# Kernel optimization log

Hardware: AMD Instinct MI355X
Metric: run time of the kernel (lower is better)

The kernel has to match this reference:

```python
import jax, jax.numpy as jnp
import numpy as np

NUM_WIRES = 12
NUM_LAYERS = 4
NUM_OUTPUTS = 4
BATCH = 1024
DIM = 2 ** NUM_WIRES


def _apply_1q(psi, U, w):
    # psi: (B, 2**n) complex64; U: (2,2) shared or (B,2,2) per-sample; wire 0 = most significant.
    B = psi.shape[0]
    L = 2 ** w
    R = DIM // (2 * L)
    psi = psi.reshape(B, L, 2, R)
    if U.ndim == 2:
        psi = jnp.einsum('ij,bljr->blir', U, psi)
    else:
        psi = jnp.einsum('bij,bljr->blir', U, psi)
    return psi.reshape(B, DIM)


def _cnot(psi, c, t):
    # CNOT(control=c, target=t): flip target amplitudes in the control=1 half.
    B = psi.shape[0]
    psi = psi.reshape((B,) + (2,) * NUM_WIRES)
    a0 = jax.lax.index_in_dim(psi, 0, c + 1, keepdims=True)
    a1 = jax.lax.index_in_dim(psi, 1, c + 1, keepdims=True)
    a1 = jnp.flip(a1, axis=t + 1)
    psi = jnp.concatenate([a0, a1], axis=c + 1)
    return psi.reshape(B, DIM)


def _rot(phi, theta, omega):
    # PennyLane Rot(phi, theta, omega) = RZ(omega) @ RY(theta) @ RZ(phi)
    c = jnp.cos(theta / 2)
    s = jnp.sin(theta / 2)
    u00 = jnp.exp(-0.5j * (phi + omega)) * c
    u01 = -jnp.exp(0.5j * (phi - omega)) * s
    u10 = jnp.exp(-0.5j * (phi - omega)) * s
    u11 = jnp.exp(0.5j * (phi + omega)) * c
    return jnp.stack([jnp.stack([u00, u01]), jnp.stack([u10, u11])]).astype(jnp.complex64)


def _circuit(inputs, weights):
    B = inputs.shape[0]
    psi = jnp.zeros((B, DIM), jnp.complex64).at[:, 0].set(1.0)
    # AngleEmbedding with rotation 'Y': RY(pi/2 * x_w) on wire w (per-sample angles)
    theta = (jnp.pi / 2) * inputs  # (B, n)
    c = jnp.cos(theta / 2)
    s = jnp.sin(theta / 2)
    for w in range(NUM_WIRES):
        U = jnp.stack([jnp.stack([c[:, w], -s[:, w]], -1),
                       jnp.stack([s[:, w], c[:, w]], -1)], -2).astype(jnp.complex64)  # (B,2,2)
        psi = _apply_1q(psi, U, w)
    # StronglyEntanglingLayers: Rot on every wire, then ring of CNOTs with range r
    for l in range(NUM_LAYERS):
        for w in range(NUM_WIRES):
            psi = _apply_1q(psi, _rot(weights[l, w, 0], weights[l, w, 1], weights[l, w, 2]), w)
        r = (l % (NUM_WIRES - 1)) + 1
        for w in range(NUM_WIRES):
            psi = _cnot(psi, w, (w + r) % NUM_WIRES)
    # expval(PauliZ) on the first NUM_OUTPUTS wires
    probs = jnp.abs(psi) ** 2  # (B, DIM) float32
    idx = jnp.arange(DIM)
    shifts = NUM_WIRES - 1 - jnp.arange(NUM_OUTPUTS)
    signs = (1.0 - 2.0 * ((idx[None, :] >> shifts[:, None]) & 1)).astype(probs.dtype)  # (NOUT, DIM)
    return probs @ signs.T  # (B, NUM_OUTPUTS)


def setup_inputs() -> dict:
    key = jax.random.key(0)
    k1, k2 = jax.random.split(key)
    inputs = jax.random.uniform(k1, (BATCH, NUM_WIRES), jnp.float32, -1.0, 1.0)
    weights = jax.random.uniform(k2, (NUM_LAYERS, NUM_WIRES, 3), jnp.float32, 0.0, 2.0 * np.pi)
    return {"inputs": inputs, "weights": weights}


def reference(inputs, weights):
    return _circuit(inputs, weights)
```

## Files before the change

kernel.cpp:

```cpp
#include <hip/hip_runtime.h>
#include <hip/hip_bf16.h>

#define NW 12
#define DIM 4096
#define NL 4
#define NGATE 48
#define NOUT 4
#define TPB 256

typedef float f32x2 __attribute__((ext_vector_type(2)));
typedef float f32x4 __attribute__((ext_vector_type(4)));
typedef unsigned u32x4 __attribute__((ext_vector_type(4)));
typedef short short8 __attribute__((ext_vector_type(8)));

constexpr int pcnt(unsigned x){ return __builtin_popcount(x); }
constexpr int msbp(unsigned x){ return x ? 31-__builtin_clz(x) : -1; }
constexpr unsigned ring_fwd(unsigned x,int r){
  for(int w=0;w<NW;++w){ int c=NW-1-w,t=NW-1-((w+r)%NW); x^=((x>>c)&1u)<<t; } return x;
}
constexpr unsigned ring_rev(unsigned x,int r){
  for(int w=NW-1;w>=0;--w){ int c=NW-1-w,t=NW-1-((w+r)%NW); x^=((x>>c)&1u)<<t; } return x;
}
struct Mat { unsigned col[12]; };
constexpr unsigned apply_cols(const Mat&M, unsigned v){
  unsigned r=0; for(int j=0;j<12;++j) if((v>>j)&1u) r^=M.col[j]; return r;
}
constexpr unsigned apply_rows(const unsigned* rows, unsigned v){
  unsigned r=0; for(int i=0;i<12;++i) r|=(unsigned)(pcnt(rows[i]&v)&1)<<i; return r;
}
constexpr bool invert_rows(const Mat&M, unsigned* ri_out){
  unsigned rb[12]={}, ri[12]={};
  for(int i=0;i<12;++i){ unsigned r=0; for(int j=0;j<12;++j) r|=((M.col[j]>>i)&1u)<<j; rb[i]=r; ri[i]=1u<<i; }
  for(int c=0;c<12;++c){
    int piv=-1; for(int r=c;r<12;++r) if((rb[r]>>c)&1u){piv=r;break;}
    if(piv<0) return false;
    unsigned t=rb[c]; rb[c]=rb[piv]; rb[piv]=t; t=ri[c]; ri[c]=ri[piv]; ri[piv]=t;
    for(int r=0;r<12;++r) if(r!=c&&((rb[r]>>c)&1u)){ rb[r]^=rb[c]; ri[r]^=ri[c]; }
  }
  for(int i=0;i<12;++i) ri_out[i]=ri[i];
  return true;
}
constexpr int nullspace4(const unsigned* A0, unsigned* out){
  unsigned A[4]={}; for(int i=0;i<4;++i) A[i]=A0[i];
  int rank=0; int pivc[4]={-1,-1,-1,-1};
  for(int c=0;c<12&&rank<4;++c){
    int piv=-1; for(int r=rank;r<4;++r) if((A[r]>>c)&1u){piv=r;break;}
    if(piv<0) continue;
    unsigned t=A[rank];A[rank]=A[piv];A[piv]=t;
    for(int r=0;r<4;++r) if(r!=rank&&((A[r]>>c)&1u)) A[r]^=A[rank];
    pivc[rank]=c; ++rank;
  }
  if(rank!=4) return -1;
  bool ispiv[12]={};
  for(int r=0;r<4;++r) ispiv[pivc[r]]=true;
  int cnt=0;
  for(int f=0;f<12;++f) if(!ispiv[f]){
    unsigned v=1u<<f;
    for(int r=0;r<4;++r) if((A[r]>>f)&1u) v|=1u<<pivc[r];
    out[cnt++]=v;
  }
  return cnt;
}
struct Ech { unsigned r[12]; int lead[12]; int n; };
constexpr unsigned ech_red(const Ech&e, unsigned v){
  int mv=msbp(v);
  for(int i=0;i<e.n&&v;++i) if(e.lead[i]==mv){ v^=e.r[i]; mv=msbp(v); }
  return v;
}
constexpr void ech_add(Ech&e, unsigned v){
  int l=msbp(v); int pos=e.n;
  while(pos>0&&e.lead[pos-1]<l){ e.r[pos]=e.r[pos-1]; e.lead[pos]=e.lead[pos-1]; --pos; }
  e.r[pos]=v; e.lead[pos]=l; e.n+=1;
}

struct Circ {
  unsigned M[NL][12]; unsigned RM[NL][12]; unsigned MR[NOUT];
};
constexpr Circ make_circ(){
  Circ C{};
  unsigned cols[12]={}, icols[12]={};
  for(int p=0;p<12;++p){ cols[p]=1u<<p; icols[p]=1u<<p; }
  for(int l=0;l<NL;++l){
    for(int w=0;w<NW;++w){
      int p=NW-1-w;
      C.M[l][w]=icols[p];
      unsigned r=0; for(int j=0;j<12;++j) r|=((cols[j]>>p)&1u)<<j;
      C.RM[l][w]=r;
    }
    int rr=(l%(NW-1))+1;
    for(int j=0;j<12;++j) cols[j]=ring_fwd(cols[j],rr);
    unsigned nic[12]={};
    for(int p=0;p<12;++p){
      unsigned y=ring_rev(1u<<p,rr), v=0;
      for(int q=0;q<12;++q) if((y>>q)&1u) v^=icols[q];
      nic[p]=v;
    }
    for(int p=0;p<12;++p) icols[p]=nic[p];
  }
  for(int o=0;o<NOUT;++o){
    int p=NW-1-o; unsigned r=0;
    for(int j=0;j<12;++j) r|=((cols[j]>>p)&1u)<<j;
    C.MR[o]=r;
  }
  return C;
}

constexpr unsigned amap(unsigned v){ return (v>>8)*2048u + (v&255u)*8u; }

struct Plan2 {
  unsigned SCOLt[8];
  unsigned SK16[16];
  unsigned TM;
  unsigned WBC[12][8], WOFF[12][16];
  unsigned RBC[12][8], ROFF[12][16];
  unsigned SRt[NOUT], KP[NOUT];
  bool ok;
};

constexpr Plan2 make_plan2(){
  Plan2 P{}; P.ok=true;
  constexpr Circ C = make_circ();
  const int SIGl[8] = {0,1,2,3,10,11,6,7};
  Mat Bprev{}; for(int j=0;j<12;++j) Bprev.col[j]=1u<<j;
  for(int g=0; g<12; ++g){
    int l=g/3, j0=(g%3)*4;
    unsigned mi[4]={}, rmi[4]={};
    for(int i=0;i<4;++i){ mi[i]=C.M[l][j0+i]; rmi[i]=C.RM[l][j0+i]; }
    unsigned u[8]={};
    if(nullspace4(rmi,u)!=8){ P.ok=false; return P; }
    unsigned binv[12]={};
    if(!invert_rows(Bprev,binv)){ P.ok=false; return P; }
    for(int s=0;s<8;++s) u[s]=apply_rows(binv,u[s]);
    Mat Bg{};
    for(int j=0;j<8;++j) Bg.col[j]=apply_cols(Bprev,u[j]);
    for(int i=0;i<4;++i) Bg.col[8+i]=mi[i];
    unsigned tinv[12]={};
    if(!invert_rows(Bg,tinv)){ P.ok=false; return P; }
    for(int i=0;i<4;++i)
      for(int j=0;j<12;++j){
        int want=(j==8+i)?1:0;
        if((pcnt(Bg.col[j]&rmi[i])&1)!=want){ P.ok=false; return P; }
      }
    if(g==0){
      for(int j=0;j<8;++j) P.SCOLt[j]=Bg.col[SIGl[j]];
      for(int idx=0;idx<16;++idx){
        unsigned v=0;
        if((idx>>2)&1) v^=Bg.col[4];
        if((idx>>2)&2) v^=Bg.col[5];
        if(idx&1) v^=Bg.col[8];
        if(idx&2) v^=Bg.col[9];
        P.SK16[idx]=v; P.TM|=v;
      }
    } else {
      unsigned rk[4]={};
      for(int i=0;i<4;++i){
        rk[i]=apply_rows(binv,mi[i]);
        if(apply_cols(Bprev,rk[i])!=mi[i]){ P.ok=false; return P; }
      }
      unsigned s2b[6]={u[0],u[1],u[2],u[3],rk[2],rk[3]};
      unsigned rows[12]={}; int nr=0;
      Ech P1{},P2{},ER{};
      for(int pick=0;pick<4;++pick){
        unsigned fx=0, fy=0;
        const int b1s[6]={0,1,2,3,10,11};
        for(int ii=0;ii<6;++ii){
          unsigned f=1u<<b1s[ii];
          unsigned p1=(f&15u)|(((f>>10)&3u)<<4);
          if(ech_red(P1,p1)){ fx=f; break; }
        }
        for(int bb=0;bb<12;++bb){
          unsigned f=1u<<bb, p2=0;
          for(int i2=0;i2<6;++i2) p2|=(unsigned)(pcnt(f&s2b[i2])&1)<<i2;
          if(ech_red(P2,p2)){ fy=f; break; }
        }
        if(!fx||!fy){ P.ok=false; return P; }
        unsigned cand[3]={fx,fy,fx^fy};
        unsigned chosen=0, cp1=0, cp2=0;
        for(int ci=0; ci<3 && !chosen; ++ci){
          unsigned f=cand[ci];
          unsigned p1=(f&15u)|(((f>>10)&3u)<<4);
          unsigned p2=0; for(int i2=0;i2<6;++i2) p2|=(unsigned)(pcnt(f&s2b[i2])&1)<<i2;
          if(ech_red(P1,p1)&&ech_red(P2,p2)){ chosen=f; cp1=p1; cp2=p2; }
        }
        if(!chosen){ P.ok=false; return P; }
        { unsigned v1=ech_red(P1,cp1); ech_add(P1,v1); }
        { unsigned v2=ech_red(P2,cp2); ech_add(P2,v2); }
        { unsigned vr=ech_red(ER,chosen); if(!vr){ P.ok=false; return P; } ech_add(ER,vr); }
        rows[nr++]=chosen;
      }
      for(int bb=0;bb<12 && nr<12;++bb){
        unsigned vr=ech_red(ER,1u<<bb); if(!vr) continue;
        ech_add(ER,vr); rows[nr++]=1u<<bb;
      }
      if(nr!=12){ P.ok=false; return P; }
      unsigned PhiCol[12]={};
      for(int j=0;j<12;++j){
        unsigned v=0;
        for(int i=0;i<12;++i) v|=(unsigned)((rows[i]>>j)&1u)<<i;
        PhiCol[j]=v;
      }
      unsigned PhiM[12]={};
      for(int j=0;j<12;++j){
        unsigned src=(j<8)? u[j] : rk[j-8];
        unsigned v=0;
        for(int q2=0;q2<12;++q2) if((src>>q2)&1u) v^=PhiCol[q2];
        PhiM[j]=v;
      }
      for(int j=0;j<8;++j){
        P.WBC[g][j]=amap(PhiCol[SIGl[j]]);
        P.RBC[g][j]=amap(PhiM[SIGl[j]]);
      }
      for(int idx=0;idx<16;++idx){
        unsigned wv=0, rv=0;
        if((idx>>2)&1){ wv^=PhiCol[4]; rv^=PhiM[4]; }
        if((idx>>2)&2){ wv^=PhiCol[5]; rv^=PhiM[5]; }
        if(idx&1){ wv^=PhiCol[8]; rv^=PhiM[8]; }
        if(idx&2){ wv^=PhiCol[9]; rv^=PhiM[9]; }
        P.WOFF[g][idx]=amap(wv); P.ROFF[g][idx]=amap(rv);
      }
    }
    Bprev=Bg;
  }
  for(int o=0;o<NOUT;++o){
    unsigned sr=0;
    for(int j=0;j<12;++j) sr|=(unsigned)(pcnt(Bprev.col[j]&C.MR[o])&1)<<j;
    unsigned srt=0;
    const int SIGl2[8] = {0,1,2,3,10,11,6,7};
    for(int j=0;j<8;++j) srt|=((sr>>SIGl2[j])&1u)<<j;
    P.SRt[o]=srt;
    unsigned kp=0;
    for(int idx=0;idx<16;++idx){
      int T=idx>>2, q=idx&3;
      unsigned bit=(((sr>>4)&1u)&(unsigned)(T&1))^(((sr>>5)&1u)&(unsigned)((T>>1)&1))
                  ^(((sr>>8)&1u)&(unsigned)(q&1))^(((sr>>9)&1u)&(unsigned)((q>>1)&1));
      kp|=bit<<idx;
    }
    P.KP[o]=kp;
  }
  return P;
}

constexpr Plan2 PL2C = make_plan2();
static_assert(PL2C.ok, "plan2 failed");
__device__ constexpr Plan2 PL2 = PL2C;

__device__ __forceinline__ void gate_coeffs(const float* __restrict__ wts, int gi, float* o){
  const float* w = wts + gi*3;
  float st,ct;  sincosf(0.5f*w[1],&st,&ct);
  float sap,cap; sincosf(0.5f*(w[0]+w[2]),&sap,&cap);
  float sam,cam; sincosf(0.5f*(w[0]-w[2]),&sam,&cam);
  o[0]= cap*ct; o[1]=-sap*ct;
  o[2]=-cam*st; o[3]=-sam*st;
  o[4]= cam*st; o[5]=-sam*st;
  o[6]= cap*ct; o[7]= sap*ct;
}
__device__ __forceinline__ unsigned cvtpk(float a, float b){
  unsigned r; asm("v_cvt_pk_bf16_f32 %0, %1, %2" : "=v"(r) : "v"(a), "v"(b)); return r;
}
__device__ __forceinline__ void split2(float x, float& hf, float& lf){
  __hip_bfloat16 hb = __float2bfloat16(x);
  hf = __bfloat162float(hb);
  lf = x - hf;
}
__device__ __forceinline__ void pkhl(float x0, float x1, unsigned& hw_out, unsigned& lw_out){
  unsigned hw = cvtpk(x0, x1);
  float h0 = __uint_as_float(hw << 16);
  float h1 = __uint_as_float(hw & 0xffff0000u);
  lw_out = cvtpk(x0 - h0, x1 - h1);
  hw_out = hw;
}

__device__ __forceinline__ void do_mfma_T(const float2& v0, const float2& v1,
                                          const float2& v2, const float2& v3,
                                          const short8* AF, f32x4& cr_o, f32x4& ci_o){
  unsigned h0,l0,h1,l1;
  pkhl(v0.x, v1.x, h0, l0);
  pkhl(v2.x, v3.x, h1, l1);
  u32x4 bu; bu.x=h0; bu.y=h1; bu.z=l0; bu.w=l1;
  short8 Br = __builtin_bit_cast(short8, bu);
  pkhl(v0.y, v1.y, h0, l0);
  pkhl(v2.y, v3.y, h1, l1);
  u32x4 cu; cu.x=h0; cu.y=h1; cu.z=l0; cu.w=l1;
  short8 Bi = __builtin_bit_cast(short8, cu);
  const f32x4 z = {0.f,0.f,0.f,0.f};
  f32x4 cr = __builtin_amdgcn_mfma_f32_16x16x32_bf16(AF[0], Br, z, 0,0,0);
  cr = __builtin_amdgcn_mfma_f32_16x16x32_bf16(AF[1], Br, cr, 0,0,0);
  cr = __builtin_amdgcn_mfma_f32_16x16x32_bf16(AF[4], Bi, cr, 0,0,0);
  cr = __builtin_amdgcn_mfma_f32_16x16x32_bf16(AF[5], Bi, cr, 0,0,0);
  f32x4 ci = __builtin_amdgcn_mfma_f32_16x16x32_bf16(AF[2], Br, z, 0,0,0);
  ci = __builtin_amdgcn_mfma_f32_16x16x32_bf16(AF[3], Br, ci, 0,0,0);
  ci = __builtin_amdgcn_mfma_f32_16x16x32_bf16(AF[0], Bi, ci, 0,0,0);
  ci = __builtin_amdgcn_mfma_f32_16x16x32_bf16(AF[1], Bi, ci, 0,0,0);
  cr_o = cr; ci_o = ci;
}

__global__ void coeff2_kernel(const float* __restrict__ wts, unsigned short* __restrict__ gfrag){
  const int g = blockIdx.x;
  const int tid = threadIdx.x;
  const int m = tid & 15, rp = tid >> 4;
  const int s = rp >> 1, reg = rp & 1;
  const int r0 = 4*s + 2*reg, r1 = r0 + 1;
  const int l = g/3, j0 = (g%3)*4;
  float ur0=1.f, ui0=0.f, ur1=1.f, ui1=0.f;
  #pragma unroll
  for(int i=0;i<4;++i){
    float o[8]; gate_coeffs(wts, l*NW + j0 + i, o);
    int mb=(m>>i)&1, rb0=(r0>>i)&1, rb1=(r1>>i)&1;
    float er=o[(mb*2+rb0)*2], ei=o[(mb*2+rb0)*2+1];
    float tr=ur0*er-ui0*ei, ti=ur0*ei+ui0*er; ur0=tr; ui0=ti;
    er=o[(mb*2+rb1)*2]; ei=o[(mb*2+rb1)*2+1];
    tr=ur1*er-ui1*ei; ti=ur1*ei+ui1*er; ur1=tr; ui1=ti;
  }
  float ur0h,ur0l,ur1h,ur1l, ui0h,ui0l,ui1h,ui1l;
  split2(ur0,ur0h,ur0l); split2(ur1,ur1h,ur1l);
  split2(ui0,ui0h,ui0l); split2(ui1,ui1h,ui1l);
  unsigned Urh=cvtpk(ur0h,ur1h), Url=cvtpk(ur0l,ur1l);
  unsigned Uih=cvtpk(ui0h,ui1h), Uil=cvtpk(ui0l,ui1l);
  unsigned nUih=Uih^0x80008000u, nUil=Uil^0x80008000u;
  const int lane = s*16 + m;
  unsigned p0[6]={Urh,Url,Uih,Uil,nUih,nUil};
  unsigned p1[6]={Url,Urh,Uil,Uih,nUil,nUih};
  #pragma unroll
  for(int f=0; f<6; ++f){
    unsigned* fp = (unsigned*)((char*)gfrag + ((size_t)((g*6+f)*64 + lane))*16);
    fp[reg] = p0[f];
    fp[2+reg] = p1[f];
  }
}

#define LUT_BYTES (11*32*8)
__global__ __launch_bounds__(TPB,4)
void vqc_mfma(const float* __restrict__ inp, const unsigned short* __restrict__ gfrag,
              float* __restrict__ out){
  __shared__ __align__(16) char smem[DIM*8 + LUT_BYTES];
  float* cs = (float*)smem; float* ss = cs+NW; float* red = cs+2*NW;
  char* ampc = smem;
  uint2* blut = (uint2*)(smem + DIM*8);
  const int t = threadIdx.x, b = blockIdx.x, l = t&63;
  if(t < NW){
    float x = inp[b*NW+t];
    float s,c; sincosf(0.78539816339744830962f*x,&s,&c);
    cs[t]=c; ss[t]=s;
  }
  for(int e=t; e<11*32; e+=TPB){
    int gg=(e>>5)+1, idx=e&31;
    int hi=idx>>4, nib=idx&15;
    unsigned wv=0, rv=0;
    #pragma unroll
    for(int j=0;j<4;++j){
      if((nib>>j)&1){
        int jj = j + (hi?4:0);
        wv ^= PL2.WBC[gg][jj];
        rv ^= PL2.RBC[gg][jj];
      }
    }
    blut[e]=make_uint2(wv,rv);
  }
  __syncthreads();
  float ctm[12], stm[12];
  #pragma unroll
  for(int p=0;p<12;++p){ ctm[p]=cs[11-p]; stm[p]=ss[11-p]; }
  unsigned sigb=0;
  #pragma unroll
  for(int j=0;j<8;++j) sigb ^= ((t>>j)&1u)? PL2.SCOLt[j] : 0u;
  float pbase=1.f;
  #pragma unroll
  for(int p=0;p<12;++p)
    if(!((PL2C.TM>>p)&1u))
      pbase *= ((sigb>>p)&1u)? stm[p] : ctm[p];

  short8 AF[6];
  #pragma unroll
  for(int f=0; f<6; ++f)
    AF[f] = *(const short8*)((const char*)gfrag + ((size_t)(f*64 + l))*16);

  f32x4 Cr[4], Ci[4];

  {
    #pragma unroll
    for(int T=0;T<4;++T){
      float vv[4];
      #pragma unroll
      for(int rq=0;rq<4;++rq){
        unsigned sig = sigb ^ PL2.SK16[T*4+rq];
        float pk=pbase;
        #pragma unroll
        for(int p=0;p<12;++p)
          if((PL2C.TM>>p)&1u)
            pk *= ((sig>>p)&1u)? stm[p] : ctm[p];
        vv[rq]=pk;
      }
      float2 v0=make_float2(vv[0],0.f), v1=make_float2(vv[1],0.f);
      float2 v2=make_float2(vv[2],0.f), v3=make_float2(vv[3],0.f);
      __builtin_amdgcn_s_setprio(1);
      do_mfma_T(v0,v1,v2,v3, AF, Cr[T], Ci[T]);
      __builtin_amdgcn_s_setprio(0);
    }
    #pragma unroll
    for(int f=0; f<6; ++f)
      AF[f] = *(const short8*)((const char*)gfrag + ((size_t)((6+f)*64 + l))*16);
  }

  #pragma unroll 1
  for(int g=1; g<12; ++g){
    const uint2* bl = blut + (g-1)*32;
    uint2 lo = bl[t&15];
    uint2 hi = bl[16 + (t>>4)];
    unsigned wbase = lo.x ^ hi.x;
    unsigned rbase = lo.y ^ hi.y;
    __syncthreads();
    #pragma unroll
    for(int idx=0; idx<16; ++idx){
      const int T=idx>>2, q=idx&3;
      *(float2*)(ampc + (wbase ^ PL2.WOFF[g][idx])) = make_float2(Cr[T][q], Ci[T][q]);
    }
    __syncthreads();
    #pragma unroll
    for(int T=0;T<4;++T){
      float2 v0 = *(const float2*)(ampc + (rbase ^ PL2.ROFF[g][T*4+0]));
      float2 v1 = *(const float2*)(ampc + (rbase ^ PL2.ROFF[g][T*4+1]));
      float2 v2 = *(const float2*)(ampc + (rbase ^ PL2.ROFF[g][T*4+2]));
      float2 v3 = *(const float2*)(ampc + (rbase ^ PL2.ROFF[g][T*4+3]));
      __builtin_amdgcn_s_setprio(1);
      do_mfma_T(v0,v1,v2,v3, AF, Cr[T], Ci[T]);
      __builtin_amdgcn_s_setprio(0);
    }
    if(g<11){
      #pragma unroll
      for(int f=0; f<6; ++f)
        AF[f] = *(const short8*)((const char*)gfrag + ((size_t)(((g+1)*6+f)*64 + l))*16);
    }
  }

  float acc[NOUT]={0.f,0.f,0.f,0.f};
  float sg[NOUT];
  #pragma unroll
  for(int o=0;o<NOUT;++o)
    sg[o] = (__popc((unsigned)t & PL2.SRt[o])&1)? -1.f : 1.f;
  #pragma unroll
  for(int idx=0; idx<16; ++idx){
    const int T=idx>>2, q=idx&3;
    float pr = Cr[T][q]*Cr[T][q] + Ci[T][q]*Ci[T][q];
    #pragma unroll
    for(int o=0;o<NOUT;++o){
      const bool kp = (PL2C.KP[o]>>idx)&1;
      float f = sg[o]*pr;
      acc[o] += kp? -f : f;
    }
  }
  #pragma unroll
  for(int o=0;o<NOUT;++o)
    #pragma unroll
    for(int off=32; off>0; off>>=1)
      acc[o] += __shfl_down(acc[o], off);
  __syncthreads();
  const int wv=t>>6, ln=t&63;
  if(ln==0){
    #pragma unroll
    for(int o=0;o<NOUT;++o) red[wv*NOUT+o]=acc[o];
  }
  __syncthreads();
  if(t<NOUT)
    out[b*NOUT+t] = red[0*NOUT+t]+red[1*NOUT+t]+red[2*NOUT+t]+red[3*NOUT+t];
}

extern "C" void kernel_launch(void* const* d_in, const int* in_sizes, int n_in,
                              void* d_out, int out_size, void* d_ws, size_t ws_size,
                              hipStream_t stream) {
  const float* inp=(const float*)d_in[0];
  const float* wts=(const float*)d_in[1];
  float* outp=(float*)d_out;
  const int B = in_sizes[0]/NW;
  unsigned short* gfrag=(unsigned short*)d_ws;
  coeff2_kernel<<<12,128,0,stream>>>(wts,gfrag);
  vqc_mfma<<<B,TPB,0,stream>>>(inp,gfrag,outp);
}
```

Measured before the change: 39.74 us.

## Double threads per sample so each thread holds 8 amplitudes instead of 16

Raises the block size from 256 to 512 threads and remaps the state-vector partition so each thread owns 8 amplitudes (2 MFMA tiles) instead of 16. The constexpr plan tables gain a ninth thread-index column and shrink the per-thread offset tables. The LDS address map becomes linear, which drops the previous bank-spreading layout, and the cached cos/sin register arrays are removed. This aims for more parallelism and fewer registers per thread, at the cost of more waves per block and more barrier participants per gate group.

```diff
diff --git a/kernel.cpp b/kernel.cpp
--- a/kernel.cpp
+++ b/kernel.cpp
@@ -6,7 +6,7 @@
 #define NL 4
 #define NGATE 48
 #define NOUT 4
-#define TPB 256
+#define TPB 512
 
 typedef float f32x2 __attribute__((ext_vector_type(2)));
 typedef float f32x4 __attribute__((ext_vector_type(4)));
@@ -105,14 +105,15 @@
   return C;
 }
 
-constexpr unsigned amap(unsigned v){ return (v>>8)*2048u + (v&255u)*8u; }
+
+constexpr unsigned amap(unsigned v){ return v*8u; }
 
 struct Plan2 {
-  unsigned SCOLt[8];
-  unsigned SK16[16];
+  unsigned SCOLt[9];
+  unsigned SK8[8];
   unsigned TM;
-  unsigned WBC[12][8], WOFF[12][16];
-  unsigned RBC[12][8], ROFF[12][16];
+  unsigned WBC[12][9], WOFF[12][8];
+  unsigned RBC[12][9], ROFF[12][8];
   unsigned SRt[NOUT], KP[NOUT];
   bool ok;
 };
@@ -120,7 +121,7 @@
 constexpr Plan2 make_plan2(){
   Plan2 P{}; P.ok=true;
   constexpr Circ C = make_circ();
-  const int SIGl[8] = {0,1,2,3,10,11,6,7};
+  const int SIGp[9] = {0,1,2,3,10,11,5,6,7};
   Mat Bprev{}; for(int j=0;j<12;++j) Bprev.col[j]=1u<<j;
   for(int g=0; g<12; ++g){
     int l=g/3, j0=(g%3)*4;
@@ -142,14 +143,13 @@
         if((pcnt(Bg.col[j]&rmi[i])&1)!=want){ P.ok=false; return P; }
       }
     if(g==0){
-      for(int j=0;j<8;++j) P.SCOLt[j]=Bg.col[SIGl[j]];
-      for(int idx=0;idx<16;++idx){
+      for(int j=0;j<9;++j) P.SCOLt[j]=Bg.col[SIGp[j]];
+      for(int idx=0;idx<8;++idx){
         unsigned v=0;
-        if((idx>>2)&1) v^=Bg.col[4];
-        if((idx>>2)&2) v^=Bg.col[5];
-        if(idx&1) v^=Bg.col[8];
-        if(idx&2) v^=Bg.col[9];
-        P.SK16[idx]=v; P.TM|=v;
+        if(idx&1) v^=Bg.col[4];
+        if(idx&2) v^=Bg.col[8];
+        if(idx&4) v^=Bg.col[9];
+        P.SK8[idx]=v; P.TM|=v;
       }
     } else {
       unsigned rk[4]={};
@@ -206,16 +206,15 @@
         for(int q2=0;q2<12;++q2) if((src>>q2)&1u) v^=PhiCol[q2];
         PhiM[j]=v;
       }
-      for(int j=0;j<8;++j){
-        P.WBC[g][j]=amap(PhiCol[SIGl[j]]);
-        P.RBC[g][j]=amap(PhiM[SIGl[j]]);
-      }
-      for(int idx=0;idx<16;++idx){
+      for(int j=0;j<9;++j){
+        P.WBC[g][j]=amap(PhiCol[SIGp[j]]);
+        P.RBC[g][j]=amap(PhiM[SIGp[j]]);
+      }
+      for(int idx=0;idx<8;++idx){
         unsigned wv=0, rv=0;
-        if((idx>>2)&1){ wv^=PhiCol[4]; rv^=PhiM[4]; }
-        if((idx>>2)&2){ wv^=PhiCol[5]; rv^=PhiM[5]; }
-        if(idx&1){ wv^=PhiCol[8]; rv^=PhiM[8]; }
-        if(idx&2){ wv^=PhiCol[9]; rv^=PhiM[9]; }
+        if(idx&1){ wv^=PhiCol[4]; rv^=PhiM[4]; }
+        if(idx&2){ wv^=PhiCol[8]; rv^=PhiM[8]; }
+        if(idx&4){ wv^=PhiCol[9]; rv^=PhiM[9]; }
         P.WOFF[g][idx]=amap(wv); P.ROFF[g][idx]=amap(rv);
       }
     }
@@ -225,14 +224,15 @@
     unsigned sr=0;
     for(int j=0;j<12;++j) sr|=(unsigned)(pcnt(Bprev.col[j]&C.MR[o])&1)<<j;
     unsigned srt=0;
-    const int SIGl2[8] = {0,1,2,3,10,11,6,7};
-    for(int j=0;j<8;++j) srt|=((sr>>SIGl2[j])&1u)<<j;
+    const int SIGp2[9] = {0,1,2,3,10,11,5,6,7};
+    for(int j=0;j<9;++j) srt|=((sr>>SIGp2[j])&1u)<<j;
     P.SRt[o]=srt;
     unsigned kp=0;
-    for(int idx=0;idx<16;++idx){
-      int T=idx>>2, q=idx&3;
-      unsigned bit=(((sr>>4)&1u)&(unsigned)(T&1))^(((sr>>5)&1u)&(unsigned)((T>>1)&1))
-                  ^(((sr>>8)&1u)&(unsigned)(q&1))^(((sr>>9)&1u)&(unsigned)((q>>1)&1));
+    for(int idx=0;idx<8;++idx){
+      int T=idx&1, q=idx>>1;
+      unsigned bit = (((sr>>4)&1u)&(unsigned)T)
+                   ^ (((sr>>8)&1u)&(unsigned)(q&1))
+                   ^ (((sr>>9)&1u)&(unsigned)((q>>1)&1));
       kp|=bit<<idx;
     }
     P.KP[o]=kp;
@@ -269,7 +269,6 @@
   lw_out = cvtpk(x0 - h0, x1 - h1);
   hw_out = hw;
 }
-
 __device__ __forceinline__ void do_mfma_T(const float2& v0, const float2& v1,
                                           const float2& v2, const float2& v3,
                                           const short8* AF, f32x4& cr_o, f32x4& ci_o){
@@ -329,7 +328,7 @@
 }
 
 #define LUT_BYTES (11*32*8)
-__global__ __launch_bounds__(TPB,4)
+__global__ __launch_bounds__(TPB,8)
 void vqc_mfma(const float* __restrict__ inp, const unsigned short* __restrict__ gfrag,
               float* __restrict__ out){
   __shared__ __align__(16) char smem[DIM*8 + LUT_BYTES];
@@ -357,38 +356,35 @@
     blut[e]=make_uint2(wv,rv);
   }
   __syncthreads();
-  float ctm[12], stm[12];
-  #pragma unroll
-  for(int p=0;p<12;++p){ ctm[p]=cs[11-p]; stm[p]=ss[11-p]; }
   unsigned sigb=0;
   #pragma unroll
-  for(int j=0;j<8;++j) sigb ^= ((t>>j)&1u)? PL2.SCOLt[j] : 0u;
+  for(int j=0;j<9;++j) sigb ^= ((t>>j)&1u)? PL2.SCOLt[j] : 0u;
   float pbase=1.f;
   #pragma unroll
   for(int p=0;p<12;++p)
     if(!((PL2C.TM>>p)&1u))
-      pbase *= ((sigb>>p)&1u)? stm[p] : ctm[p];
+      pbase *= ((sigb>>p)&1u)? ss[11-p] : cs[11-p];
 
   short8 AF[6];
   #pragma unroll
   for(int f=0; f<6; ++f)
     AF[f] = *(const short8*)((const char*)gfrag + ((size_t)(f*64 + l))*16);
 
-  f32x4 Cr[4], Ci[4];
+  f32x4 Cr[2], Ci[2];
 
   {
     #pragma unroll
-    for(int T=0;T<4;++T){
+    for(int T=0;T<2;++T){
       float vv[4];
       #pragma unroll
-      for(int rq=0;rq<4;++rq){
-        unsigned sig = sigb ^ PL2.SK16[T*4+rq];
+      for(int q=0;q<4;++q){
+        unsigned sig = sigb ^ PL2.SK8[T | (q<<1)];
         float pk=pbase;
         #pragma unroll
         for(int p=0;p<12;++p)
           if((PL2C.TM>>p)&1u)
-            pk *= ((sig>>p)&1u)? stm[p] : ctm[p];
-        vv[rq]=pk;
+            pk *= ((sig>>p)&1u)? ss[11-p] : cs[11-p];
+        vv[q]=pk;
       }
       float2 v0=make_float2(vv[0],0.f), v1=make_float2(vv[1],0.f);
       float2 v2=make_float2(vv[2],0.f), v3=make_float2(vv[3],0.f);
@@ -405,22 +401,26 @@
   for(int g=1; g<12; ++g){
     const uint2* bl = blut + (g-1)*32;
     uint2 lo = bl[t&15];
-    uint2 hi = bl[16 + (t>>4)];
+    uint2 hi = bl[16 + ((t>>4)&15)];
     unsigned wbase = lo.x ^ hi.x;
     unsigned rbase = lo.y ^ hi.y;
+    if(t & 256){
+      wbase ^= PL2.WBC[g][8];
+      rbase ^= PL2.RBC[g][8];
+    }
     __syncthreads();
     #pragma unroll
-    for(int idx=0; idx<16; ++idx){
-      const int T=idx>>2, q=idx&3;
+    for(int idx=0; idx<8; ++idx){
+      const int T=idx&1, q=idx>>1;
       *(float2*)(ampc + (wbase ^ PL2.WOFF[g][idx])) = make_float2(Cr[T][q], Ci[T][q]);
     }
     __syncthreads();
     #pragma unroll
-    for(int T=0;T<4;++T){
-      float2 v0 = *(const float2*)(ampc + (rbase ^ PL2.ROFF[g][T*4+0]));
-      float2 v1 = *(const float2*)(ampc + (rbase ^ PL2.ROFF[g][T*4+1]));
-      float2 v2 = *(const float2*)(ampc + (rbase ^ PL2.ROFF[g][T*4+2]));
-      float2 v3 = *(const float2*)(ampc + (rbase ^ PL2.ROFF[g][T*4+3]));
+    for(int T=0;T<2;++T){
+      float2 v0 = *(const float2*)(ampc + (rbase ^ PL2.ROFF[g][(0<<1)|T]));
+      float2 v1 = *(const float2*)(ampc + (rbase ^ PL2.ROFF[g][(1<<1)|T]));
+      float2 v2 = *(const float2*)(ampc + (rbase ^ PL2.ROFF[g][(2<<1)|T]));
+      float2 v3 = *(const float2*)(ampc + (rbase ^ PL2.ROFF[g][(3<<1)|T]));
       __builtin_amdgcn_s_setprio(1);
       do_mfma_T(v0,v1,v2,v3, AF, Cr[T], Ci[T]);
       __builtin_amdgcn_s_setprio(0);
@@ -438,8 +438,8 @@
   for(int o=0;o<NOUT;++o)
     sg[o] = (__popc((unsigned)t & PL2.SRt[o])&1)? -1.f : 1.f;
   #pragma unroll
-  for(int idx=0; idx<16; ++idx){
-    const int T=idx>>2, q=idx&3;
+  for(int idx=0; idx<8; ++idx){
+    const int T=idx&1, q=idx>>1;
     float pr = Cr[T][q]*Cr[T][q] + Ci[T][q]*Ci[T][q];
     #pragma unroll
     for(int o=0;o<NOUT;++o){
@@ -460,8 +460,12 @@
     for(int o=0;o<NOUT;++o) red[wv*NOUT+o]=acc[o];
   }
   __syncthreads();
-  if(t<NOUT)
-    out[b*NOUT+t] = red[0*NOUT+t]+red[1*NOUT+t]+red[2*NOUT+t]+red[3*NOUT+t];
+  if(t<NOUT){
+    float s=0.f;
+    #pragma unroll
+    for(int w=0;w<8;++w) s += red[w*NOUT+t];
+    out[b*NOUT+t] = s;
+  }
 }
 
 extern "C" void kernel_launch(void* const* d_in, const int* in_sizes, int n_in,
```

Result: slower. 43.15 us (+8.6%).

## Process two batch samples per block to share gate fragments and overlap MFMA chains

Applied to the files above, without the earlier changes.

Each block now simulates two samples with separate LDS amplitude buffers, interleaving their shuffles and MFMA chains. Gate fragments loaded from global memory are reused across both samples, and one barrier per gate is removed. The cost is double the registers and LDS per block, lowered launch bounds, and half as many blocks, which reduces how many waves are in flight.

```diff
diff --git a/kernel.cpp b/kernel.cpp
--- a/kernel.cpp
+++ b/kernel.cpp
@@ -269,7 +269,6 @@
   lw_out = cvtpk(x0 - h0, x1 - h1);
   hw_out = hw;
 }
-
 __device__ __forceinline__ void do_mfma_T(const float2& v0, const float2& v1,
                                           const float2& v2, const float2& v3,
                                           const short8* AF, f32x4& cr_o, f32x4& ci_o){
@@ -329,18 +328,25 @@
 }
 
 #define LUT_BYTES (11*32*8)
-__global__ __launch_bounds__(TPB,4)
+__global__ __launch_bounds__(TPB,2)
 void vqc_mfma(const float* __restrict__ inp, const unsigned short* __restrict__ gfrag,
               float* __restrict__ out){
-  __shared__ __align__(16) char smem[DIM*8 + LUT_BYTES];
-  float* cs = (float*)smem; float* ss = cs+NW; float* red = cs+2*NW;
-  char* ampc = smem;
-  uint2* blut = (uint2*)(smem + DIM*8);
+  __shared__ __align__(16) char smem[2*DIM*8 + LUT_BYTES];
+  __shared__ float csb[2][NW], ssb[2][NW];
+  __shared__ float red[2][4][NOUT];
+  char* ampA = smem;
+  char* ampB = smem + DIM*8;
+  uint2* blut = (uint2*)(smem + 2*DIM*8);
   const int t = threadIdx.x, b = blockIdx.x, l = t&63;
   if(t < NW){
-    float x = inp[b*NW+t];
+    float x = inp[(2*b)*NW+t];
     float s,c; sincosf(0.78539816339744830962f*x,&s,&c);
-    cs[t]=c; ss[t]=s;
+    csb[0][t]=c; ssb[0][t]=s;
+  } else if(t >= 64 && t < 64+NW){
+    int tt = t-64;
+    float x = inp[(2*b+1)*NW+tt];
+    float s,c; sincosf(0.78539816339744830962f*x,&s,&c);
+    csb[1][tt]=c; ssb[1][tt]=s;
   }
   for(int e=t; e<11*32; e+=TPB){
     int gg=(e>>5)+1, idx=e&31;
@@ -357,26 +363,24 @@
     blut[e]=make_uint2(wv,rv);
   }
   __syncthreads();
-  float ctm[12], stm[12];
-  #pragma unroll
-  for(int p=0;p<12;++p){ ctm[p]=cs[11-p]; stm[p]=ss[11-p]; }
   unsigned sigb=0;
   #pragma unroll
   for(int j=0;j<8;++j) sigb ^= ((t>>j)&1u)? PL2.SCOLt[j] : 0u;
-  float pbase=1.f;
-  #pragma unroll
-  for(int p=0;p<12;++p)
-    if(!((PL2C.TM>>p)&1u))
-      pbase *= ((sigb>>p)&1u)? stm[p] : ctm[p];
 
   short8 AF[6];
   #pragma unroll
   for(int f=0; f<6; ++f)
     AF[f] = *(const short8*)((const char*)gfrag + ((size_t)(f*64 + l))*16);
 
-  f32x4 Cr[4], Ci[4];
-
-  {
+  f32x4 CrA[4], CiA[4], CrB[4], CiB[4];
+
+  #pragma unroll
+  for(int s=0; s<2; ++s){
+    float pbase=1.f;
+    #pragma unroll
+    for(int p=0;p<12;++p)
+      if(!((PL2C.TM>>p)&1u))
+        pbase *= ((sigb>>p)&1u)? ssb[s][11-p] : csb[s][11-p];
     #pragma unroll
     for(int T=0;T<4;++T){
       float vv[4];
@@ -387,19 +391,20 @@
         #pragma unroll
         for(int p=0;p<12;++p)
           if((PL2C.TM>>p)&1u)
-            pk *= ((sig>>p)&1u)? stm[p] : ctm[p];
+            pk *= ((sig>>p)&1u)? ssb[s][11-p] : csb[s][11-p];
         vv[rq]=pk;
       }
       float2 v0=make_float2(vv[0],0.f), v1=make_float2(vv[1],0.f);
       float2 v2=make_float2(vv[2],0.f), v3=make_float2(vv[3],0.f);
       __builtin_amdgcn_s_setprio(1);
-      do_mfma_T(v0,v1,v2,v3, AF, Cr[T], Ci[T]);
+      if(s==0) do_mfma_T(v0,v1,v2,v3, AF, CrA[T], CiA[T]);
+      else     do_mfma_T(v0,v1,v2,v3, AF, CrB[T], CiB[T]);
       __builtin_amdgcn_s_setprio(0);
     }
-    #pragma unroll
-    for(int f=0; f<6; ++f)
-      AF[f] = *(const short8*)((const char*)gfrag + ((size_t)((6+f)*64 + l))*16);
-  }
+  }
+  #pragma unroll
+  for(int f=0; f<6; ++f)
+    AF[f] = *(const short8*)((const char*)gfrag + ((size_t)((6+f)*64 + l))*16);
 
   #pragma unroll 1
   for(int g=1; g<12; ++g){
@@ -408,21 +413,36 @@
     uint2 hi = bl[16 + (t>>4)];
     unsigned wbase = lo.x ^ hi.x;
     unsigned rbase = lo.y ^ hi.y;
-    __syncthreads();
     #pragma unroll
     for(int idx=0; idx<16; ++idx){
       const int T=idx>>2, q=idx&3;
-      *(float2*)(ampc + (wbase ^ PL2.WOFF[g][idx])) = make_float2(Cr[T][q], Ci[T][q]);
+      *(float2*)(ampA + (wbase ^ PL2.WOFF[g][idx])) = make_float2(CrA[T][q], CiA[T][q]);
     }
     __syncthreads();
+    float2 ra[16];
+    #pragma unroll
+    for(int idx=0; idx<16; ++idx)
+      ra[idx] = *(const float2*)(ampA + (rbase ^ PL2.ROFF[g][idx]));
+    #pragma unroll
+    for(int idx=0; idx<16; ++idx){
+      const int T=idx>>2, q=idx&3;
+      *(float2*)(ampB + (wbase ^ PL2.WOFF[g][idx])) = make_float2(CrB[T][q], CiB[T][q]);
+    }
+    __syncthreads();
+    float2 rb[16];
+    #pragma unroll
+    for(int idx=0; idx<16; ++idx)
+      rb[idx] = *(const float2*)(ampB + (rbase ^ PL2.ROFF[g][idx]));
     #pragma unroll
     for(int T=0;T<4;++T){
-      float2 v0 = *(const float2*)(ampc + (rbase ^ PL2.ROFF[g][T*4+0]));
-      float2 v1 = *(const float2*)(ampc + (rbase ^ PL2.ROFF[g][T*4+1]));
-      float2 v2 = *(const float2*)(ampc + (rbase ^ PL2.ROFF[g][T*4+2]));
-      float2 v3 = *(const float2*)(ampc + (rbase ^ PL2.ROFF[g][T*4+3]));
       __builtin_amdgcn_s_setprio(1);
-      do_mfma_T(v0,v1,v2,v3, AF, Cr[T], Ci[T]);
+      do_mfma_T(ra[T*4+0], ra[T*4+1], ra[T*4+2], ra[T*4+3], AF, CrA[T], CiA[T]);
+      __builtin_amdgcn_s_setprio(0);
+    }
+    #pragma unroll
+    for(int T=0;T<4;++T){
+      __builtin_amdgcn_s_setprio(1);
+      do_mfma_T(rb[T*4+0], rb[T*4+1], rb[T*4+2], rb[T*4+3], AF, CrB[T], CiB[T]);
       __builtin_amdgcn_s_setprio(0);
     }
     if(g<11){
@@ -432,36 +452,40 @@
     }
   }
 
-  float acc[NOUT]={0.f,0.f,0.f,0.f};
   float sg[NOUT];
   #pragma unroll
   for(int o=0;o<NOUT;++o)
     sg[o] = (__popc((unsigned)t & PL2.SRt[o])&1)? -1.f : 1.f;
+  float accA[NOUT]={0,0,0,0}, accB[NOUT]={0,0,0,0};
   #pragma unroll
   for(int idx=0; idx<16; ++idx){
     const int T=idx>>2, q=idx&3;
-    float pr = Cr[T][q]*Cr[T][q] + Ci[T][q]*Ci[T][q];
+    float prA = CrA[T][q]*CrA[T][q] + CiA[T][q]*CiA[T][q];
+    float prB = CrB[T][q]*CrB[T][q] + CiB[T][q]*CiB[T][q];
     #pragma unroll
     for(int o=0;o<NOUT;++o){
       const bool kp = (PL2C.KP[o]>>idx)&1;
-      float f = sg[o]*pr;
-      acc[o] += kp? -f : f;
+      accA[o] += kp? -sg[o]*prA : sg[o]*prA;
+      accB[o] += kp? -sg[o]*prB : sg[o]*prB;
     }
   }
   #pragma unroll
   for(int o=0;o<NOUT;++o)
     #pragma unroll
-    for(int off=32; off>0; off>>=1)
-      acc[o] += __shfl_down(acc[o], off);
-  __syncthreads();
+    for(int off=32; off>0; off>>=1){
+      accA[o] += __shfl_down(accA[o], off);
+      accB[o] += __shfl_down(accB[o], off);
+    }
   const int wv=t>>6, ln=t&63;
   if(ln==0){
     #pragma unroll
-    for(int o=0;o<NOUT;++o) red[wv*NOUT+o]=acc[o];
+    for(int o=0;o<NOUT;++o){ red[0][wv][o]=accA[o]; red[1][wv][o]=accB[o]; }
   }
   __syncthreads();
-  if(t<NOUT)
-    out[b*NOUT+t] = red[0*NOUT+t]+red[1*NOUT+t]+red[2*NOUT+t]+red[3*NOUT+t];
+  if(t<NOUT){
+    out[(2*b)*NOUT+t]   = red[0][0][t]+red[0][1][t]+red[0][2][t]+red[0][3][t];
+    out[(2*b+1)*NOUT+t] = red[1][0][t]+red[1][1][t]+red[1][2][t]+red[1][3][t];
+  }
 }
 
 extern "C" void kernel_launch(void* const* d_in, const int* in_sizes, int n_in,
@@ -473,5 +497,5 @@
   const int B = in_sizes[0]/NW;
   unsigned short* gfrag=(unsigned short*)d_ws;
   coeff2_kernel<<<12,128,0,stream>>>(wts,gfrag);
-  vqc_mfma<<<B,TPB,0,stream>>>(inp,gfrag,outp);
-}
+  vqc_mfma<<<B/2,TPB,0,stream>>>(inp,gfrag,outp);
+}
```

Result: slower. 40.83 us (+2.7%).
